# Performance work log

Hardware: AMD Instinct MI355X
Metric: run time of the kernel (lower is better)

The kernel has to match this reference:

```python
import jax, jax.numpy as jnp
import numpy as np

B, S, E = 8, 4096, 256
NQ, F = 8, 1024


def setup_inputs() -> dict:
    key = jax.random.key(0)
    k1, k2, k3, k4 = jax.random.split(key, 4)
    x = jax.random.normal(k1, (B, S, E), dtype=jnp.float32)
    theta = jax.random.normal(k2, (NQ,), dtype=jnp.float32)
    W1 = jax.random.normal(k3, (F, NQ), dtype=jnp.float32) * (1.0 / np.sqrt(NQ))
    W2 = jax.random.normal(k4, (E, F), dtype=jnp.float32) * (1.0 / np.sqrt(F))
    return {"x": x, "theta": theta, "W1": W1, "W2": W2}


def reference(x, theta, W1, W2):
    # Quantum layer: per wire w, |0> -> RX(x_w) -> RY(theta_w) -> <Z>.
    # No entangling gates => product state; exact closed form:
    #   <Z_w> = cos(x_w) * cos(theta_w)
    nq = theta.shape[0]
    q = jnp.cos(x[..., :nq]) * jnp.cos(theta)           # [B, S, nq]
    # dropout is identity in eval mode (p interpreted at inference)
    h = jax.nn.relu(jnp.einsum('bsq,fq->bsf', q, W1))   # [B, S, F]
    return jnp.einsum('bsf,ef->bse', h, W2)             # [B, S, E]
```

## Files before the change

kernel.cpp:

```cpp
#include <hip/hip_runtime.h>
#include <hip/hip_bf16.h>

typedef __attribute__((ext_vector_type(8))) short  short8_t;
typedef __attribute__((ext_vector_type(4))) float  float4_t;
typedef __attribute__((ext_vector_type(4))) int    int4_t;
typedef __attribute__((ext_vector_type(2))) unsigned int uint2_t;

__device__ __forceinline__ unsigned short f2bf(float f) {
    unsigned int u = __builtin_bit_cast(unsigned int, f);
    u += 0x7FFFu + ((u >> 16) & 1u);
    return (unsigned short)(u >> 16);
}
__device__ __forceinline__ unsigned int cvtpk(float a, float b) {
    return (unsigned int)f2bf(a) | ((unsigned int)f2bf(b) << 16);
}
__device__ __forceinline__ unsigned int cvtpk_hw(float a, float b) {
    unsigned int r;
    asm("v_cvt_pk_bf16_f32 %0, %1, %2" : "=v"(r) : "v"(a), "v"(b));
    return r;
}
__device__ __forceinline__ void plane32_swap(unsigned int& a, unsigned int& b) {
    asm("v_permlane32_swap_b32 %0, %1" : "+v"(a), "+v"(b));
}
__device__ __forceinline__ void plane16_swap(unsigned int& a, unsigned int& b) {
    asm("v_permlane16_swap_b32 %0, %1" : "+v"(a), "+v"(b));
}
__device__ __forceinline__ void gld16(int4_t& d, const void* p) {
    asm volatile("global_load_dwordx4 %0, %1, off" : "=&v"(d) : "v"(p) : "memory");
}
__device__ __forceinline__ void wait12() {
    asm volatile("s_waitcnt vmcnt(12)" ::: "memory");
    __builtin_amdgcn_sched_barrier(0);
}
__device__ __forceinline__ void wait_all() {
    asm volatile("s_waitcnt vmcnt(0)" ::: "memory");
    __builtin_amdgcn_sched_barrier(0);
}

#define W1ROWS 1088

__global__ void prep_kernel(const float* __restrict__ W2, const float* __restrict__ W1,
                            unsigned short* __restrict__ W2s, unsigned short* __restrict__ W1b) {
    const int bid = blockIdx.x, tid = threadIdx.x;
    if (bid < 128) {
        const int idx = bid * 256 + tid;
        const int e   = idx >> 7;
        const int ks  = idx & 127;
        const float* src = W2 + (size_t)e * 1024 + ks * 8;
        const float4_t v0 = *reinterpret_cast<const float4_t*>(src);
        const float4_t v1 = *reinterpret_cast<const float4_t*>(src + 4);
        int4_t p;
        p[0] = (int)cvtpk(v0[0], v0[1]);
        p[1] = (int)cvtpk(v0[2], v0[3]);
        p[2] = (int)cvtpk(v1[0], v1[1]);
        p[3] = (int)cvtpk(v1[2], v1[3]);
        *reinterpret_cast<int4_t*>(W2s + ((size_t)ks * 256 + e) * 8) = p;
    } else {
        const int base = tid * 32;
        #pragma unroll
        for (int it = 0; it < 8; ++it) {
            const float4_t v = *reinterpret_cast<const float4_t*>(W1 + base + it * 4);
            uint2_t p;
            p[0] = cvtpk(v[0], v[1]);
            p[1] = cvtpk(v[2], v[3]);
            *reinterpret_cast<uint2_t*>(W1b + base + it * 4) = p;
        }
        if (tid < 16) {
            #pragma unroll
            for (int it = 0; it < 4; ++it) {
                int4_t z; z[0] = 0; z[1] = 0; z[2] = 0; z[3] = 0;
                *reinterpret_cast<int4_t*>(W1b + 8192 + tid * 32 + it * 8) = z;
            }
        }
    }
}

template <bool WSOK>
__global__ __launch_bounds__(256, 2)
void ffq_kernel(const float* __restrict__ x,
                const float* __restrict__ theta,
                const float* __restrict__ W1f,
                const unsigned short* __restrict__ W1b,
                const float* __restrict__ W2f,
                const unsigned short* __restrict__ W2s,
                float* __restrict__ out)
{
    const int tid  = threadIdx.x;
    const int lane = tid & 63;
    const int w    = tid >> 6;
    const int bid  = blockIdx.x;
    const int ntile   = bid & 3;
    const int rowbase = (bid >> 2) * 256 + w * 64;
    const int colbase = ntile * 64;
    const int lr = lane & 15;
    const int G  = lane >> 4;

    short8_t qf[4];
    #pragma unroll
    for (int mt = 0; mt < 4; ++mt) {
        short8_t v = {0,0,0,0,0,0,0,0};
        if (lane < 16) {
            const float* xp = x + (size_t)(rowbase + mt * 16 + lane) * 256;
            const float4_t x0 = *reinterpret_cast<const float4_t*>(xp);
            const float4_t x1 = *reinterpret_cast<const float4_t*>(xp + 4);
            float qv[8];
            #pragma unroll
            for (int j = 0; j < 4; ++j) {
                qv[j]     = __cosf(x0[j]) * __cosf(theta[j]);
                qv[4 + j] = __cosf(x1[j]) * __cosf(theta[4 + j]);
            }
            int4_t pq;
            pq[0] = (int)cvtpk(qv[0], qv[1]);
            pq[1] = (int)cvtpk(qv[2], qv[3]);
            pq[2] = (int)cvtpk(qv[4], qv[5]);
            pq[3] = (int)cvtpk(qv[6], qv[7]);
            v = __builtin_bit_cast(short8_t, pq);
        }
        qf[mt] = v;
    }

    float4_t acc[4][4];
    #pragma unroll
    for (int i = 0; i < 4; ++i)
        #pragma unroll
        for (int j = 0; j < 4; ++j)
            acc[i][j] = (float4_t){0.f, 0.f, 0.f, 0.f};

    auto compute = [&](const int4_t& a0, const int4_t& a1,
                       const int4_t& b0, const int4_t& b1,
                       const int4_t& b2, const int4_t& b3) {
        const short8_t af0 = __builtin_bit_cast(short8_t, a0);
        const short8_t af1 = __builtin_bit_cast(short8_t, a1);
        short8_t afrag[4];
        #pragma unroll
        for (int mt = 0; mt < 4; ++mt) {
            const float4_t t0 = __builtin_amdgcn_mfma_f32_16x16x32_bf16(
                af0, qf[mt], (float4_t){0.f, 0.f, 0.f, 0.f}, 0, 0, 0);
            const float4_t t1 = __builtin_amdgcn_mfma_f32_16x16x32_bf16(
                af1, qf[mt], (float4_t){0.f, 0.f, 0.f, 0.f}, 0, 0, 0);
            unsigned int A_ = cvtpk_hw(fmaxf(t0[0], 0.f), fmaxf(t0[1], 0.f));
            unsigned int B_ = cvtpk_hw(fmaxf(t0[2], 0.f), fmaxf(t0[3], 0.f));
            unsigned int C_ = cvtpk_hw(fmaxf(t1[0], 0.f), fmaxf(t1[1], 0.f));
            unsigned int D_ = cvtpk_hw(fmaxf(t1[2], 0.f), fmaxf(t1[3], 0.f));
            plane32_swap(A_, C_);
            plane16_swap(A_, C_);
            plane32_swap(B_, D_);
            plane16_swap(B_, D_);
            int4_t ua;
            ua[0] = (int)A_; ua[1] = (int)B_; ua[2] = (int)C_; ua[3] = (int)D_;
            afrag[mt] = __builtin_bit_cast(short8_t, ua);
        }
        const short8_t bfr[4] = {
            __builtin_bit_cast(short8_t, b0), __builtin_bit_cast(short8_t, b1),
            __builtin_bit_cast(short8_t, b2), __builtin_bit_cast(short8_t, b3) };
        #pragma unroll
        for (int mt = 0; mt < 4; ++mt)
            #pragma unroll
            for (int cf = 0; cf < 4; ++cf)
                acc[mt][cf] = __builtin_amdgcn_mfma_f32_16x16x32_bf16(
                    afrag[mt], bfr[cf], acc[mt][cf], 0, 0, 0);
    };

    if constexpr (WSOK) {
        auto a_addr = [&](int kc, int t) -> const void* {
            return (const void*)(W1b + (size_t)(kc + t * 16 + lane) * 8);
        };
        auto b_addr = [&](int kc, int cf) -> const void* {
            const int e = colbase + cf * 16 + lr;
            return (const void*)(W2s + (((size_t)(kc >> 3) + G) * 256 + e) * 8);
        };
        int4_t Aa0, Aa1, Ab0, Ab1, Ab2, Ab3;
        int4_t Ba0, Ba1, Bb0, Bb1, Bb2, Bb3;
        int4_t Ca0, Ca1, Cb0, Cb1, Cb2, Cb3;
        int4_t Da0, Da1, Db0, Db1, Db2, Db3;

        #define ISSUE(P, K) do { const int kk_ = (K) & 1023;              \
            gld16(P##a0, a_addr(kk_, 0)); gld16(P##a1, a_addr(kk_, 1));   \
            gld16(P##b0, b_addr(kk_, 0)); gld16(P##b1, b_addr(kk_, 1));   \
            gld16(P##b2, b_addr(kk_, 2)); gld16(P##b3, b_addr(kk_, 3)); } while (0)
        #define COMPUTE(P) compute(P##a0, P##a1, P##b0, P##b1, P##b2, P##b3)

        ISSUE(A, 0);
        ISSUE(B, 32);
        #pragma unroll 1
        for (int kc = 0; kc < 1024; kc += 128) {
            ISSUE(C, kc + 64);  wait12(); COMPUTE(A);
            ISSUE(D, kc + 96);  wait12(); COMPUTE(B);
            ISSUE(A, kc + 128); wait12(); COMPUTE(C);
            ISSUE(B, kc + 160); wait12(); COMPUTE(D);
        }
        wait_all();
        #undef ISSUE
        #undef COMPUTE
    } else {
        for (int kc = 0; kc < 1024; kc += 32) {
            int4_t a0 = {0,0,0,0}, a1 = {0,0,0,0};
            if (lane < 16) {
                #pragma unroll
                for (int t = 0; t < 2; ++t) {
                    const float* src = W1f + (size_t)(kc + t * 16 + lane) * 8;
                    const float4_t v0 = *reinterpret_cast<const float4_t*>(src);
                    const float4_t v1 = *reinterpret_cast<const float4_t*>(src + 4);
                    int4_t p;
                    p[0] = (int)cvtpk(v0[0], v0[1]);
                    p[1] = (int)cvtpk(v0[2], v0[3]);
                    p[2] = (int)cvtpk(v1[0], v1[1]);
                    p[3] = (int)cvtpk(v1[2], v1[3]);
                    if (t == 0) a0 = p; else a1 = p;
                }
            }
            int4_t b[4];
            #pragma unroll
            for (int cf = 0; cf < 4; ++cf) {
                const int e = colbase + cf * 16 + lr;
                const float* p = W2f + (size_t)e * 1024 + kc + G * 8;
                const float4_t v0 = *reinterpret_cast<const float4_t*>(p);
                const float4_t v1 = *reinterpret_cast<const float4_t*>(p + 4);
                int4_t pb;
                pb[0] = (int)cvtpk(v0[0], v0[1]);
                pb[1] = (int)cvtpk(v0[2], v0[3]);
                pb[2] = (int)cvtpk(v1[0], v1[1]);
                pb[3] = (int)cvtpk(v1[2], v1[3]);
                b[cf] = pb;
            }
            compute(a0, a1, b[0], b[1], b[2], b[3]);
        }
    }

    #pragma unroll
    for (int mt = 0; mt < 4; ++mt)
        #pragma unroll
        for (int cf = 0; cf < 4; ++cf)
            #pragma unroll
            for (int r = 0; r < 4; ++r) {
                const int gr = rowbase + mt * 16 + G * 4 + r;
                const int gc = colbase + cf * 16 + lr;
                out[(size_t)gr * 256 + gc] = acc[mt][cf][r];
            }
}

extern "C" void kernel_launch(void* const* d_in, const int* in_sizes, int n_in,
                              void* d_out, int out_size, void* d_ws, size_t ws_size,
                              hipStream_t stream) {
    const float* x     = (const float*)d_in[0];
    const float* theta = (const float*)d_in[1];
    const float* W1    = (const float*)d_in[2];
    const float* W2    = (const float*)d_in[3];
    float* out = (float*)d_out;

    const size_t need = (size_t)(256 * 1024 + W1ROWS * 8) * sizeof(unsigned short);
    const bool wsok = (ws_size >= need);

    if (wsok) {
        unsigned short* W2s = (unsigned short*)d_ws;
        unsigned short* W1b = W2s + 256 * 1024;
        prep_kernel<<<129, 256, 0, stream>>>(W2, W1, W2s, W1b);
        ffq_kernel<true><<<512, 256, 0, stream>>>(x, theta, nullptr, W1b, nullptr, W2s, out);
    } else {
        ffq_kernel<false><<<512, 256, 0, stream>>>(x, theta, W1, nullptr, W2, nullptr, out);
    }
}
```

Measured before the change: 40.75 us.

## Compute hidden layer once per row block via LDS, shrink tile to 16 rows

Each block now covers 16 rows and all 256 output columns. Its four waves each compute a 256-wide slice of the ReLU hidden activations exactly once and stage them in shared memory. The old scheme recomputed the first GEMM for every 64-column output tile. After a barrier, each wave streams W2 fragments from global memory and reads the hidden fragments from LDS. In exchange, each W2 load now feeds only one MFMA instead of four, which multiplies L2 traffic for W2, and occupancy rises to 4 blocks per CU with a 2048-block grid.

```diff
diff --git a/kernel.cpp b/kernel.cpp
--- a/kernel.cpp
+++ b/kernel.cpp
@@ -19,17 +19,11 @@
     asm("v_cvt_pk_bf16_f32 %0, %1, %2" : "=v"(r) : "v"(a), "v"(b));
     return r;
 }
-__device__ __forceinline__ void plane32_swap(unsigned int& a, unsigned int& b) {
-    asm("v_permlane32_swap_b32 %0, %1" : "+v"(a), "+v"(b));
-}
-__device__ __forceinline__ void plane16_swap(unsigned int& a, unsigned int& b) {
-    asm("v_permlane16_swap_b32 %0, %1" : "+v"(a), "+v"(b));
-}
 __device__ __forceinline__ void gld16(int4_t& d, const void* p) {
     asm volatile("global_load_dwordx4 %0, %1, off" : "=&v"(d) : "v"(p) : "memory");
 }
-__device__ __forceinline__ void wait12() {
-    asm volatile("s_waitcnt vmcnt(12)" ::: "memory");
+__device__ __forceinline__ void wait8() {
+    asm volatile("s_waitcnt vmcnt(8)" ::: "memory");
     __builtin_amdgcn_sched_barrier(0);
 }
 __device__ __forceinline__ void wait_all() {
@@ -76,7 +70,7 @@
 }
 
 template <bool WSOK>
-__global__ __launch_bounds__(256, 2)
+__global__ __launch_bounds__(256, 4)
 void ffq_kernel(const float* __restrict__ x,
                 const float* __restrict__ theta,
                 const float* __restrict__ W1f,
@@ -85,131 +79,109 @@
                 const unsigned short* __restrict__ W2s,
                 float* __restrict__ out)
 {
+    __shared__ __align__(16) unsigned short h_lds[128][16][8];
+
     const int tid  = threadIdx.x;
     const int lane = tid & 63;
     const int w    = tid >> 6;
     const int bid  = blockIdx.x;
-    const int ntile   = bid & 3;
-    const int rowbase = (bid >> 2) * 256 + w * 64;
-    const int colbase = ntile * 64;
+    const int rowbase = bid * 16;
+    const int colbase = w * 64;
     const int lr = lane & 15;
     const int G  = lane >> 4;
 
-    short8_t qf[4];
+    short8_t qf = {0,0,0,0,0,0,0,0};
+    if (lane < 16) {
+        const float* xp = x + (size_t)(rowbase + lane) * 256;
+        const float4_t x0 = *reinterpret_cast<const float4_t*>(xp);
+        const float4_t x1 = *reinterpret_cast<const float4_t*>(xp + 4);
+        float qv[8];
+        #pragma unroll
+        for (int j = 0; j < 4; ++j) {
+            qv[j]     = __cosf(x0[j]) * __cosf(theta[j]);
+            qv[4 + j] = __cosf(x1[j]) * __cosf(theta[4 + j]);
+        }
+        int4_t pq;
+        pq[0] = (int)cvtpk(qv[0], qv[1]);
+        pq[1] = (int)cvtpk(qv[2], qv[3]);
+        pq[2] = (int)cvtpk(qv[4], qv[5]);
+        pq[3] = (int)cvtpk(qv[6], qv[7]);
+        qf = __builtin_bit_cast(short8_t, pq);
+    }
+
     #pragma unroll
-    for (int mt = 0; mt < 4; ++mt) {
-        short8_t v = {0,0,0,0,0,0,0,0};
-        if (lane < 16) {
-            const float* xp = x + (size_t)(rowbase + mt * 16 + lane) * 256;
-            const float4_t x0 = *reinterpret_cast<const float4_t*>(xp);
-            const float4_t x1 = *reinterpret_cast<const float4_t*>(xp + 4);
-            float qv[8];
-            #pragma unroll
-            for (int j = 0; j < 4; ++j) {
-                qv[j]     = __cosf(x0[j]) * __cosf(theta[j]);
-                qv[4 + j] = __cosf(x1[j]) * __cosf(theta[4 + j]);
-            }
-            int4_t pq;
-            pq[0] = (int)cvtpk(qv[0], qv[1]);
-            pq[1] = (int)cvtpk(qv[2], qv[3]);
-            pq[2] = (int)cvtpk(qv[4], qv[5]);
-            pq[3] = (int)cvtpk(qv[6], qv[7]);
-            v = __builtin_bit_cast(short8_t, pq);
-        }
-        qf[mt] = v;
-    }
-
-    float4_t acc[4][4];
+    for (int ft = 0; ft < 16; ++ft) {
+        const int fg = w * 16 + ft;
+        short8_t af;
+        if constexpr (WSOK) {
+            af = *reinterpret_cast<const short8_t*>(W1b + ((size_t)(fg * 16 + lr) * 8 + G * 8));
+        } else {
+            const float* src = W1f + (size_t)(fg * 16 + lr) * 8;
+            const float4_t v0 = *reinterpret_cast<const float4_t*>(src);
+            const float4_t v1 = *reinterpret_cast<const float4_t*>(src + 4);
+            int4_t p;
+            p[0] = (int)cvtpk(v0[0], v0[1]);
+            p[1] = (int)cvtpk(v0[2], v0[3]);
+            p[2] = (int)cvtpk(v1[0], v1[1]);
+            p[3] = (int)cvtpk(v1[2], v1[3]);
+            af = __builtin_bit_cast(short8_t, p);
+        }
+        const float4_t d = __builtin_amdgcn_mfma_f32_16x16x32_bf16(
+            af, qf, (float4_t){0.f, 0.f, 0.f, 0.f}, 0, 0, 0);
+        uint2_t pk;
+        pk[0] = cvtpk_hw(fmaxf(d[0], 0.f), fmaxf(d[1], 0.f));
+        pk[1] = cvtpk_hw(fmaxf(d[2], 0.f), fmaxf(d[3], 0.f));
+        *reinterpret_cast<uint2_t*>(&h_lds[2 * fg + (G >> 1)][lr][(G & 1) * 4]) = pk;
+    }
+
+    __syncthreads();
+
+    float4_t acc[4];
     #pragma unroll
-    for (int i = 0; i < 4; ++i)
-        #pragma unroll
-        for (int j = 0; j < 4; ++j)
-            acc[i][j] = (float4_t){0.f, 0.f, 0.f, 0.f};
-
-    auto compute = [&](const int4_t& a0, const int4_t& a1,
-                       const int4_t& b0, const int4_t& b1,
-                       const int4_t& b2, const int4_t& b3) {
-        const short8_t af0 = __builtin_bit_cast(short8_t, a0);
-        const short8_t af1 = __builtin_bit_cast(short8_t, a1);
-        short8_t afrag[4];
-        #pragma unroll
-        for (int mt = 0; mt < 4; ++mt) {
-            const float4_t t0 = __builtin_amdgcn_mfma_f32_16x16x32_bf16(
-                af0, qf[mt], (float4_t){0.f, 0.f, 0.f, 0.f}, 0, 0, 0);
-            const float4_t t1 = __builtin_amdgcn_mfma_f32_16x16x32_bf16(
-                af1, qf[mt], (float4_t){0.f, 0.f, 0.f, 0.f}, 0, 0, 0);
-            unsigned int A_ = cvtpk_hw(fmaxf(t0[0], 0.f), fmaxf(t0[1], 0.f));
-            unsigned int B_ = cvtpk_hw(fmaxf(t0[2], 0.f), fmaxf(t0[3], 0.f));
-            unsigned int C_ = cvtpk_hw(fmaxf(t1[0], 0.f), fmaxf(t1[1], 0.f));
-            unsigned int D_ = cvtpk_hw(fmaxf(t1[2], 0.f), fmaxf(t1[3], 0.f));
-            plane32_swap(A_, C_);
-            plane16_swap(A_, C_);
-            plane32_swap(B_, D_);
-            plane16_swap(B_, D_);
-            int4_t ua;
-            ua[0] = (int)A_; ua[1] = (int)B_; ua[2] = (int)C_; ua[3] = (int)D_;
-            afrag[mt] = __builtin_bit_cast(short8_t, ua);
-        }
-        const short8_t bfr[4] = {
-            __builtin_bit_cast(short8_t, b0), __builtin_bit_cast(short8_t, b1),
-            __builtin_bit_cast(short8_t, b2), __builtin_bit_cast(short8_t, b3) };
-        #pragma unroll
-        for (int mt = 0; mt < 4; ++mt)
-            #pragma unroll
-            for (int cf = 0; cf < 4; ++cf)
-                acc[mt][cf] = __builtin_amdgcn_mfma_f32_16x16x32_bf16(
-                    afrag[mt], bfr[cf], acc[mt][cf], 0, 0, 0);
-    };
+    for (int j = 0; j < 4; ++j) acc[j] = (float4_t){0.f, 0.f, 0.f, 0.f};
 
     if constexpr (WSOK) {
-        auto a_addr = [&](int kc, int t) -> const void* {
-            return (const void*)(W1b + (size_t)(kc + t * 16 + lane) * 8);
-        };
         auto b_addr = [&](int kc, int cf) -> const void* {
             const int e = colbase + cf * 16 + lr;
             return (const void*)(W2s + (((size_t)(kc >> 3) + G) * 256 + e) * 8);
         };
-        int4_t Aa0, Aa1, Ab0, Ab1, Ab2, Ab3;
-        int4_t Ba0, Ba1, Bb0, Bb1, Bb2, Bb3;
-        int4_t Ca0, Ca1, Cb0, Cb1, Cb2, Cb3;
-        int4_t Da0, Da1, Db0, Db1, Db2, Db3;
-
-        #define ISSUE(P, K) do { const int kk_ = (K) & 1023;              \
-            gld16(P##a0, a_addr(kk_, 0)); gld16(P##a1, a_addr(kk_, 1));   \
-            gld16(P##b0, b_addr(kk_, 0)); gld16(P##b1, b_addr(kk_, 1));   \
+        int4_t Ab0, Ab1, Ab2, Ab3;
+        int4_t Bb0, Bb1, Bb2, Bb3;
+        int4_t Cb0, Cb1, Cb2, Cb3;
+        int4_t Db0, Db1, Db2, Db3;
+
+        #define ISSUE(P, K) do { const int kk_ = (K) & 1023;                \
+            gld16(P##b0, b_addr(kk_, 0)); gld16(P##b1, b_addr(kk_, 1));     \
             gld16(P##b2, b_addr(kk_, 2)); gld16(P##b3, b_addr(kk_, 3)); } while (0)
-        #define COMPUTE(P) compute(P##a0, P##a1, P##b0, P##b1, P##b2, P##b3)
-
+        #define COMPUTE(P, KC) do {                                                      \
+            const short8_t afu = afn;                                                    \
+            afn = *reinterpret_cast<const short8_t*>(                                    \
+                &h_lds[((((KC) + 32) & 1023) >> 3) + G][lr][0]);                         \
+            acc[0] = __builtin_amdgcn_mfma_f32_16x16x32_bf16(                            \
+                afu, __builtin_bit_cast(short8_t, P##b0), acc[0], 0, 0, 0);              \
+            acc[1] = __builtin_amdgcn_mfma_f32_16x16x32_bf16(                            \
+                afu, __builtin_bit_cast(short8_t, P##b1), acc[1], 0, 0, 0);              \
+            acc[2] = __builtin_amdgcn_mfma_f32_16x16x32_bf16(                            \
+                afu, __builtin_bit_cast(short8_t, P##b2), acc[2], 0, 0, 0);              \
+            acc[3] = __builtin_amdgcn_mfma_f32_16x16x32_bf16(                            \
+                afu, __builtin_bit_cast(short8_t, P##b3), acc[3], 0, 0, 0); } while (0)
+
+        short8_t afn = *reinterpret_cast<const short8_t*>(&h_lds[G][lr][0]);
         ISSUE(A, 0);
         ISSUE(B, 32);
         #pragma unroll 1
         for (int kc = 0; kc < 1024; kc += 128) {
-            ISSUE(C, kc + 64);  wait12(); COMPUTE(A);
-            ISSUE(D, kc + 96);  wait12(); COMPUTE(B);
-            ISSUE(A, kc + 128); wait12(); COMPUTE(C);
-            ISSUE(B, kc + 160); wait12(); COMPUTE(D);
+            ISSUE(C, kc + 64);  wait8(); COMPUTE(A, kc);
+            ISSUE(D, kc + 96);  wait8(); COMPUTE(B, kc + 32);
+            ISSUE(A, kc + 128); wait8(); COMPUTE(C, kc + 64);
+            ISSUE(B, kc + 160); wait8(); COMPUTE(D, kc + 96);
         }
         wait_all();
         #undef ISSUE
         #undef COMPUTE
     } else {
         for (int kc = 0; kc < 1024; kc += 32) {
-            int4_t a0 = {0,0,0,0}, a1 = {0,0,0,0};
-            if (lane < 16) {
-                #pragma unroll
-                for (int t = 0; t < 2; ++t) {
-                    const float* src = W1f + (size_t)(kc + t * 16 + lane) * 8;
-                    const float4_t v0 = *reinterpret_cast<const float4_t*>(src);
-                    const float4_t v1 = *reinterpret_cast<const float4_t*>(src + 4);
-                    int4_t p;
-                    p[0] = (int)cvtpk(v0[0], v0[1]);
-                    p[1] = (int)cvtpk(v0[2], v0[3]);
-                    p[2] = (int)cvtpk(v1[0], v1[1]);
-                    p[3] = (int)cvtpk(v1[2], v1[3]);
-                    if (t == 0) a0 = p; else a1 = p;
-                }
-            }
-            int4_t b[4];
+            const short8_t af = *reinterpret_cast<const short8_t*>(&h_lds[(kc >> 3) + G][lr][0]);
             #pragma unroll
             for (int cf = 0; cf < 4; ++cf) {
                 const int e = colbase + cf * 16 + lr;
@@ -221,22 +193,20 @@
                 pb[1] = (int)cvtpk(v0[2], v0[3]);
                 pb[2] = (int)cvtpk(v1[0], v1[1]);
                 pb[3] = (int)cvtpk(v1[2], v1[3]);
-                b[cf] = pb;
+                acc[cf] = __builtin_amdgcn_mfma_f32_16x16x32_bf16(
+                    af, __builtin_bit_cast(short8_t, pb), acc[cf], 0, 0, 0);
             }
-            compute(a0, a1, b[0], b[1], b[2], b[3]);
         }
     }
 
     #pragma unroll
-    for (int mt = 0; mt < 4; ++mt)
+    for (int cf = 0; cf < 4; ++cf)
         #pragma unroll
-        for (int cf = 0; cf < 4; ++cf)
-            #pragma unroll
-            for (int r = 0; r < 4; ++r) {
-                const int gr = rowbase + mt * 16 + G * 4 + r;
-                const int gc = colbase + cf * 16 + lr;
-                out[(size_t)gr * 256 + gc] = acc[mt][cf][r];
-            }
+        for (int r = 0; r < 4; ++r) {
+            const int gr = rowbase + G * 4 + r;
+            const int gc = colbase + cf * 16 + lr;
+            out[(size_t)gr * 256 + gc] = acc[cf][r];
+        }
 }
 
 extern "C" void kernel_launch(void* const* d_in, const int* in_sizes, int n_in,
@@ -255,8 +225,8 @@
         unsigned short* W2s = (unsigned short*)d_ws;
         unsigned short* W1b = W2s + 256 * 1024;
         prep_kernel<<<129, 256, 0, stream>>>(W2, W1, W2s, W1b);
-        ffq_kernel<true><<<512, 256, 0, stream>>>(x, theta, nullptr, W1b, nullptr, W2s, out);
+        ffq_kernel<true><<<2048, 256, 0, stream>>>(x, theta, nullptr, W1b, nullptr, W2s, out);
     } else {
-        ffq_kernel<false><<<512, 256, 0, stream>>>(x, theta, W1, nullptr, W2, nullptr, out);
-    }
-}
+        ffq_kernel<false><<<2048, 256, 0, stream>>>(x, theta, W1, nullptr, W2, nullptr, out);
+    }
+}
```

Measured after the change: 52.79 us. 29.6% more time.

## Split K across warp pairs with LDS reduction and double the grid

Applied to the files above, without the earlier changes.

Each block now pairs warps that split the 1024-wide hidden dimension in halves. The second warp of each pair writes its partial accumulators to shared memory, and the first adds them before storing output. The grid doubles to 1024 blocks and launch bounds rise to 3 blocks per CU, which raises parallelism and occupancy. The prefetch pipeline is restructured to separate the hidden-chunk compute from the main MFMA, with a shallower vmcnt wait. The cost is a shared-memory reduction plus a barrier, about 33KB of LDS per block, and an extra padded W1 tail for overrun prefetches.

```diff
diff --git a/kernel.cpp b/kernel.cpp
--- a/kernel.cpp
+++ b/kernel.cpp
@@ -28,8 +28,8 @@
 __device__ __forceinline__ void gld16(int4_t& d, const void* p) {
     asm volatile("global_load_dwordx4 %0, %1, off" : "=&v"(d) : "v"(p) : "memory");
 }
-__device__ __forceinline__ void wait12() {
-    asm volatile("s_waitcnt vmcnt(12)" ::: "memory");
+__device__ __forceinline__ void wait6() {
+    asm volatile("s_waitcnt vmcnt(6)" ::: "memory");
     __builtin_amdgcn_sched_barrier(0);
 }
 __device__ __forceinline__ void wait_all() {
@@ -37,7 +37,7 @@
     __builtin_amdgcn_sched_barrier(0);
 }
 
-#define W1ROWS 1088
+#define W1ROWS 1152
 
 __global__ void prep_kernel(const float* __restrict__ W2, const float* __restrict__ W1,
                             unsigned short* __restrict__ W2s, unsigned short* __restrict__ W1b) {
@@ -65,7 +65,7 @@
             p[1] = cvtpk(v[2], v[3]);
             *reinterpret_cast<uint2_t*>(W1b + base + it * 4) = p;
         }
-        if (tid < 16) {
+        if (tid < 32) {
             #pragma unroll
             for (int it = 0; it < 4; ++it) {
                 int4_t z; z[0] = 0; z[1] = 0; z[2] = 0; z[3] = 0;
@@ -76,7 +76,7 @@
 }
 
 template <bool WSOK>
-__global__ __launch_bounds__(256, 2)
+__global__ __launch_bounds__(256, 3)
 void ffq_kernel(const float* __restrict__ x,
                 const float* __restrict__ theta,
                 const float* __restrict__ W1f,
@@ -85,13 +85,19 @@
                 const unsigned short* __restrict__ W2s,
                 float* __restrict__ out)
 {
+    __shared__ float red[2][64][65];
+
     const int tid  = threadIdx.x;
     const int lane = tid & 63;
     const int w    = tid >> 6;
     const int bid  = blockIdx.x;
-    const int ntile   = bid & 3;
-    const int rowbase = (bid >> 2) * 256 + w * 64;
+    const int ntile = bid & 3;
+    const int mpair = bid >> 2;
+    const int tloc  = w >> 1;
+    const int khalf = w & 1;
+    const int rowbase = (mpair * 2 + tloc) * 64;
     const int colbase = ntile * 64;
+    const int kbase   = khalf * 512;
     const int lr = lane & 15;
     const int G  = lane >> 4;
 
@@ -126,12 +132,11 @@
         for (int j = 0; j < 4; ++j)
             acc[i][j] = (float4_t){0.f, 0.f, 0.f, 0.f};
 
-    auto compute = [&](const int4_t& a0, const int4_t& a1,
-                       const int4_t& b0, const int4_t& b1,
-                       const int4_t& b2, const int4_t& b3) {
+    short8_t afrag[4];
+
+    auto hch = [&](const int4_t& a0, const int4_t& a1) {
         const short8_t af0 = __builtin_bit_cast(short8_t, a0);
         const short8_t af1 = __builtin_bit_cast(short8_t, a1);
-        short8_t afrag[4];
         #pragma unroll
         for (int mt = 0; mt < 4; ++mt) {
             const float4_t t0 = __builtin_amdgcn_mfma_f32_16x16x32_bf16(
@@ -150,6 +155,9 @@
             ua[0] = (int)A_; ua[1] = (int)B_; ua[2] = (int)C_; ua[3] = (int)D_;
             afrag[mt] = __builtin_bit_cast(short8_t, ua);
         }
+    };
+    auto mainmm = [&](const int4_t& b0, const int4_t& b1,
+                      const int4_t& b2, const int4_t& b3) {
         const short8_t bfr[4] = {
             __builtin_bit_cast(short8_t, b0), __builtin_bit_cast(short8_t, b1),
             __builtin_bit_cast(short8_t, b2), __builtin_bit_cast(short8_t, b3) };
@@ -169,31 +177,39 @@
             const int e = colbase + cf * 16 + lr;
             return (const void*)(W2s + (((size_t)(kc >> 3) + G) * 256 + e) * 8);
         };
-        int4_t Aa0, Aa1, Ab0, Ab1, Ab2, Ab3;
-        int4_t Ba0, Ba1, Bb0, Bb1, Bb2, Bb3;
-        int4_t Ca0, Ca1, Cb0, Cb1, Cb2, Cb3;
-        int4_t Da0, Da1, Db0, Db1, Db2, Db3;
-
-        #define ISSUE(P, K) do { const int kk_ = (K) & 1023;              \
-            gld16(P##a0, a_addr(kk_, 0)); gld16(P##a1, a_addr(kk_, 1));   \
-            gld16(P##b0, b_addr(kk_, 0)); gld16(P##b1, b_addr(kk_, 1));   \
+        int4_t Xa0, Xa1, Ya0, Ya1;
+        int4_t Ab0, Ab1, Ab2, Ab3;
+        int4_t Bb0, Bb1, Bb2, Bb3;
+
+        #define ISSUE_BF(P, K) do { const int kk_ = (K);                    \
+            gld16(P##b0, b_addr(kk_, 0)); gld16(P##b1, b_addr(kk_, 1));     \
             gld16(P##b2, b_addr(kk_, 2)); gld16(P##b3, b_addr(kk_, 3)); } while (0)
-        #define COMPUTE(P) compute(P##a0, P##a1, P##b0, P##b1, P##b2, P##b3)
-
-        ISSUE(A, 0);
-        ISSUE(B, 32);
+
+        gld16(Xa0, a_addr(kbase, 0)); gld16(Xa1, a_addr(kbase, 1));
+        wait_all();
+        hch(Xa0, Xa1);
+        ISSUE_BF(A, kbase);
+        gld16(Ya0, a_addr(kbase + 32, 0)); gld16(Ya1, a_addr(kbase + 32, 1));
+
         #pragma unroll 1
-        for (int kc = 0; kc < 1024; kc += 128) {
-            ISSUE(C, kc + 64);  wait12(); COMPUTE(A);
-            ISSUE(D, kc + 96);  wait12(); COMPUTE(B);
-            ISSUE(A, kc + 128); wait12(); COMPUTE(C);
-            ISSUE(B, kc + 160); wait12(); COMPUTE(D);
+        for (int it = 0; it < 8; ++it) {
+            const int c = kbase + it * 64;
+            ISSUE_BF(B, c + 32);
+            gld16(Xa0, a_addr(c + 64, 0)); gld16(Xa1, a_addr(c + 64, 1));
+            wait6();
+            mainmm(Ab0, Ab1, Ab2, Ab3);
+            hch(Ya0, Ya1);
+            ISSUE_BF(A, c + 64);
+            gld16(Ya0, a_addr(c + 96, 0)); gld16(Ya1, a_addr(c + 96, 1));
+            wait6();
+            mainmm(Bb0, Bb1, Bb2, Bb3);
+            hch(Xa0, Xa1);
         }
         wait_all();
-        #undef ISSUE
-        #undef COMPUTE
+        #undef ISSUE_BF
     } else {
-        for (int kc = 0; kc < 1024; kc += 32) {
+        for (int cc = 0; cc < 16; ++cc) {
+            const int kc = kbase + cc * 32;
             int4_t a0 = {0,0,0,0}, a1 = {0,0,0,0};
             if (lane < 16) {
                 #pragma unroll
@@ -209,6 +225,7 @@
                     if (t == 0) a0 = p; else a1 = p;
                 }
             }
+            hch(a0, a1);
             int4_t b[4];
             #pragma unroll
             for (int cf = 0; cf < 4; ++cf) {
@@ -223,20 +240,33 @@
                 pb[3] = (int)cvtpk(v1[2], v1[3]);
                 b[cf] = pb;
             }
-            compute(a0, a1, b[0], b[1], b[2], b[3]);
-        }
-    }
-
-    #pragma unroll
-    for (int mt = 0; mt < 4; ++mt)
-        #pragma unroll
-        for (int cf = 0; cf < 4; ++cf)
-            #pragma unroll
-            for (int r = 0; r < 4; ++r) {
-                const int gr = rowbase + mt * 16 + G * 4 + r;
-                const int gc = colbase + cf * 16 + lr;
-                out[(size_t)gr * 256 + gc] = acc[mt][cf][r];
-            }
+            mainmm(b[0], b[1], b[2], b[3]);
+        }
+    }
+
+    if (khalf) {
+        #pragma unroll
+        for (int mt = 0; mt < 4; ++mt)
+            #pragma unroll
+            for (int cf = 0; cf < 4; ++cf)
+                #pragma unroll
+                for (int r = 0; r < 4; ++r)
+                    red[tloc][mt * 16 + G * 4 + r][cf * 16 + lr] = acc[mt][cf][r];
+    }
+    __syncthreads();
+    if (!khalf) {
+        #pragma unroll
+        for (int mt = 0; mt < 4; ++mt)
+            #pragma unroll
+            for (int cf = 0; cf < 4; ++cf)
+                #pragma unroll
+                for (int r = 0; r < 4; ++r) {
+                    const int gr = rowbase + mt * 16 + G * 4 + r;
+                    const int gc = colbase + cf * 16 + lr;
+                    out[(size_t)gr * 256 + gc] =
+                        acc[mt][cf][r] + red[tloc][mt * 16 + G * 4 + r][cf * 16 + lr];
+                }
+    }
 }
 
 extern "C" void kernel_launch(void* const* d_in, const int* in_sizes, int n_in,
@@ -255,8 +285,8 @@
         unsigned short* W2s = (unsigned short*)d_ws;
         unsigned short* W1b = W2s + 256 * 1024;
         prep_kernel<<<129, 256, 0, stream>>>(W2, W1, W2s, W1b);
-        ffq_kernel<true><<<512, 256, 0, stream>>>(x, theta, nullptr, W1b, nullptr, W2s, out);
+        ffq_kernel<true><<<1024, 256, 0, stream>>>(x, theta, nullptr, W1b, nullptr, W2s, out);
     } else {
-        ffq_kernel<false><<<512, 256, 0, stream>>>(x, theta, W1, nullptr, W2, nullptr, out);
-    }
-}
+        ffq_kernel<false><<<1024, 256, 0, stream>>>(x, theta, W1, nullptr, W2, nullptr, out);
+    }
+}
```

Measured after the change: 39.99 us. About the same (-1.9%).
